# Performance work log

Measured on AMD Instinct MI355X. Metric: run time of the kernel, lower is better.

The kernel has to match this reference:

```python
import jax, jax.numpy as jnp
import numpy as np

B = 16          # graphs
NPG = 8192      # nodes per graph
N = B * NPG     # 131072 total nodes
E = 524288      # edges
F_NODE = 16
F_EDGE = 4
D = 128         # hidden_dim
OUT = 4
L = 3           # num_gnn_layers
K = 4096        # ceil(0.5 * NPG) nodes kept by SAGPooling
EPS = 1e-5


def setup_inputs() -> dict:
    key = jax.random.key(0)
    ks = jax.random.split(key, 24)
    # node / edge features
    x = jax.random.normal(ks[0], (N, F_NODE), jnp.float32)
    edge_attr = jax.random.normal(ks[1], (E, F_EDGE), jnp.float32)
    # edges constrained within each graph (nodes ordered by graph)
    gid = jax.random.randint(ks[2], (E,), 0, B)
    src = jax.random.randint(ks[3], (E,), 0, NPG) + gid * NPG
    dst = jax.random.randint(ks[4], (E,), 0, NPG) + gid * NPG
    edge_index = jnp.stack([src, dst]).astype(jnp.int32)

    def lin(k, fi, fo):
        kw, kb = jax.random.split(k)
        s = 1.0 / np.sqrt(fi)
        return (jax.random.uniform(kw, (fi, fo), jnp.float32, -s, s),
                jax.random.uniform(kb, (fo,), jnp.float32, -s, s))

    node_w, node_b = lin(ks[5], F_NODE, D)
    ew, eb = lin(ks[6], F_EDGE, D)
    conv_w = jax.random.normal(ks[7], (L, D, D), jnp.float32) / np.sqrt(D)
    conv_b = jnp.zeros((L, D), jnp.float32)
    bn_g = jnp.ones((L, D), jnp.float32)
    bn_b = jnp.zeros((L, D), jnp.float32)
    bn_m = jax.random.normal(ks[8], (L, D), jnp.float32) * 0.1
    bn_v = jax.random.uniform(ks[9], (L, D), jnp.float32, 0.5, 1.5)
    pool_wr, _ = lin(ks[10], D, 1)   # GraphConv lin_rel (neighbors)
    pool_ws, pool_b = lin(ks[11], D, 1)  # GraphConv lin_root (self) + bias
    r1_w, r1_b = lin(ks[12], D, D // 2)
    r2_w, r2_b = lin(ks[13], D // 2, OUT)
    return dict(x=x, edge_attr=edge_attr, edge_index=edge_index,
                node_w=node_w, node_b=node_b, ew=ew, eb=eb,
                conv_w=conv_w, conv_b=conv_b, bn_g=bn_g, bn_b=bn_b,
                bn_m=bn_m, bn_v=bn_v,
                pool_wr=pool_wr, pool_ws=pool_ws, pool_b=pool_b,
                r1_w=r1_w, r1_b=r1_b, r2_w=r2_w, r2_b=r2_b)


def reference(x, edge_attr, edge_index, node_w, node_b, ew, eb,
              conv_w, conv_b, bn_g, bn_b, bn_m, bn_v,
              pool_wr, pool_ws, pool_b, r1_w, r1_b, r2_w, r2_b):
    src, dst = edge_index[0], edge_index[1]
    # edge embedding (computed, but unused by GCNConv — faithful to source)
    _ea = jax.nn.leaky_relu(edge_attr @ ew + eb)
    h = x @ node_w + node_b                              # [N, D]
    # gcn_norm with self-loops: deg = 1 + in-degree
    deg = jax.ops.segment_sum(jnp.ones(E, h.dtype), dst, N) + 1.0
    dis = jax.lax.rsqrt(deg)                             # [N]
    coef = dis[src] * dis[dst]                           # [E]
    for i in range(L):
        hw = h @ conv_w[i]                               # [N, D]
        agg = jax.ops.segment_sum(hw[src] * coef[:, None], dst, N)
        h = agg + hw * (dis * dis)[:, None] + conv_b[i]  # GCNConv
        # BatchNorm (eval mode: running stats)
        h = (h - bn_m[i]) * jax.lax.rsqrt(bn_v[i] + EPS) * bn_g[i] + bn_b[i]
        h = jax.nn.leaky_relu(h)
        # dropout in eval mode = identity
    # SAGPooling: score via GraphConv(D, 1), aggr='add', nonlinearity=tanh
    nagg = jax.ops.segment_sum(h[src], dst, N)           # sum over neighbors
    score = (nagg @ pool_wr + h @ pool_ws + pool_b).reshape(N)
    top_vals, top_idx = jax.lax.top_k(score.reshape(B, NPG), K)  # per graph
    hb = h.reshape(B, NPG, D)
    hp = jnp.take_along_axis(hb, top_idx[..., None], axis=1)
    hp = hp * jnp.tanh(top_vals)[..., None]              # [B, K, D]
    xg = hp.sum(axis=1)                                  # global_add_pool [B, D]
    out = jax.nn.leaky_relu(xg @ r1_w + r1_b) @ r2_w + r2_b
    return out                                           # [B, OUT]
```

## Files before the change

### kernel.cpp

```cpp
#include <hip/hip_runtime.h>

#define N_NODES 131072
#define E_EDGES 524288
#define NGRAPH  16
#define NPG     8192
#define DIM     128
#define KSEL    4096
#define SCAN_BLOCKS 128

typedef float v2f __attribute__((ext_vector_type(2)));
typedef float v4f __attribute__((ext_vector_type(4)));

__global__ void count_deg_kernel(const int* __restrict__ ei, int* __restrict__ deg) {
    int e = blockIdx.x * 256 + threadIdx.x;
    atomicAdd(&deg[ei[E_EDGES + e]], 1);
}

__global__ __launch_bounds__(256) void scan_partial_kernel(const int* __restrict__ deg,
                                                           int* __restrict__ bsum) {
    __shared__ int wsh[4];
    int b = blockIdx.x, t = threadIdx.x;
    int4 v = ((const int4*)&deg[b * 1024])[t];
    int s = v.x + v.y + v.z + v.w;
#pragma unroll
    for (int off = 32; off; off >>= 1) s += __shfl_xor(s, off);
    if ((t & 63) == 0) wsh[t >> 6] = s;
    __syncthreads();
    if (t == 0) bsum[b] = wsh[0] + wsh[1] + wsh[2] + wsh[3];
}

__global__ __launch_bounds__(128) void scan_bsum_kernel(const int* __restrict__ bsum,
                                                        int* __restrict__ boff,
                                                        int* __restrict__ rowptr) {
    __shared__ int w0;
    int t = threadIdx.x;
    int lane = t & 63;
    int v = bsum[t];
    int x = v;
#pragma unroll
    for (int off = 1; off < 64; off <<= 1) {
        int y = __shfl_up(x, off);
        if (lane >= off) x += y;
    }
    if (t == 63) w0 = x;
    __syncthreads();
    int incl = x + ((t >= 64) ? w0 : 0);
    boff[t] = incl - v;
    if (t == 127) rowptr[N_NODES] = incl;
}

__global__ __launch_bounds__(256) void scan_final_kernel(const int* __restrict__ deg,
                                                         const int* __restrict__ boff,
                                                         int* __restrict__ rowptr,
                                                         int* __restrict__ cursor,
                                                         float* __restrict__ dis) {
    __shared__ int wsum[4];
    int b = blockIdx.x, t = threadIdx.x;
    int lane = t & 63, wv = t >> 6;
    int4 v = ((const int4*)&deg[b * 1024])[t];
    int s = v.x + v.y + v.z + v.w;
    int x = s;
#pragma unroll
    for (int off = 1; off < 64; off <<= 1) {
        int y = __shfl_up(x, off);
        if (lane >= off) x += y;
    }
    if (lane == 63) wsum[wv] = x;
    __syncthreads();
    int add = boff[b];
#pragma unroll
    for (int j = 0; j < 4; ++j)
        if (j < wv) add += wsum[j];
    int excl = add + (x - s);
    int base = b * 1024 + t * 4;
    int4 rp;
    rp.x = excl;
    rp.y = excl + v.x;
    rp.z = rp.y + v.y;
    rp.w = rp.z + v.z;
    *(int4*)&rowptr[base] = rp;
    *(int4*)&cursor[base] = rp;
    float4 dv;
    dv.x = rsqrtf((float)v.x + 1.0f);
    dv.y = rsqrtf((float)v.y + 1.0f);
    dv.z = rsqrtf((float)v.z + 1.0f);
    dv.w = rsqrtf((float)v.w + 1.0f);
    *(float4*)&dis[base] = dv;
}

__global__ void fill_csr_kernel(const int* __restrict__ ei, int* __restrict__ cursor,
                                const float* __restrict__ dis, int* __restrict__ csr_src,
                                float* __restrict__ csr_coef) {
    int e = blockIdx.x * 256 + threadIdx.x;
    int s = ei[e];
    int d = ei[E_EDGES + e];
    int p = atomicAdd(&cursor[d], 1);
    csr_src[p] = s;
    csr_coef[p] = dis[s] * dis[d];
}

__global__ __launch_bounds__(256) void embed_kernel(const float* __restrict__ x,
                                                    const float* __restrict__ nw,
                                                    const float* __restrict__ nb,
                                                    float* __restrict__ h) {
    __shared__ float Wl[16 * DIM];
    int t = threadIdx.x;
    for (int i = t * 4; i < 16 * DIM; i += 1024)
        *(float4*)&Wl[i] = *(const float4*)&nw[i];
    __syncthreads();
    int xslot = blockIdx.x & 7, q = blockIdx.x >> 3;
    int g = xslot + ((q >= 256) ? 8 : 0);
    int chunk = q & 255;
    int base = g * NPG + chunk * 32;
    int d = t & 127, sub = t >> 7;
    float bias = nb[d];
    for (int k = 0; k < 16; ++k) {
        int n = base + k * 2 + sub;
        const float* xr = &x[n * 16];
        float acc = bias;
#pragma unroll
        for (int f = 0; f < 16; ++f) acc += xr[f] * Wl[f * DIM + d];
        h[n * DIM + d] = acc;
    }
}

__global__ __launch_bounds__(256) void agg_kernel(const float* __restrict__ h,
                                                  const int* __restrict__ rowptr,
                                                  const int* __restrict__ csr_src,
                                                  const float* __restrict__ csr_coef,
                                                  const float* __restrict__ dis,
                                                  float* __restrict__ m) {
    int bb = blockIdx.x;
    int xslot = bb & 7;
    int c = bb >> 3;
    int g = xslot + ((c >= 512) ? 8 : 0);
    int chunk = c & 511;
    int t = threadIdx.x;
    int nl = t >> 6, l = t & 63;
    int nbase = g * NPG + chunk * 16;
#pragma unroll
    for (int it = 0; it < 4; ++it) {
        int n = nbase + it * 4 + nl;
        float dn = dis[n];
        float2 hv = *(const float2*)&h[(size_t)n * DIM + l * 2];
        float ax = dn * dn * hv.x;
        float ay = dn * dn * hv.y;
        int e0 = rowptr[n], e1 = rowptr[n + 1];
        int e = e0;
        for (; e + 4 <= e1; e += 4) {
            int s0 = csr_src[e],     s1 = csr_src[e + 1];
            int s2 = csr_src[e + 2], s3 = csr_src[e + 3];
            float c0 = csr_coef[e],     c1 = csr_coef[e + 1];
            float c2 = csr_coef[e + 2], c3 = csr_coef[e + 3];
            float2 v0 = *(const float2*)&h[(size_t)s0 * DIM + l * 2];
            float2 v1 = *(const float2*)&h[(size_t)s1 * DIM + l * 2];
            float2 v2 = *(const float2*)&h[(size_t)s2 * DIM + l * 2];
            float2 v3 = *(const float2*)&h[(size_t)s3 * DIM + l * 2];
            ax = fmaf(c0, v0.x, fmaf(c1, v1.x, fmaf(c2, v2.x, fmaf(c3, v3.x, ax))));
            ay = fmaf(c0, v0.y, fmaf(c1, v1.y, fmaf(c2, v2.y, fmaf(c3, v3.y, ay))));
        }
        for (; e < e1; ++e) {
            int s = csr_src[e];
            float cf = csr_coef[e];
            float2 v = *(const float2*)&h[(size_t)s * DIM + l * 2];
            ax = fmaf(cf, v.x, ax);
            ay = fmaf(cf, v.y, ay);
        }
        float2 o;
        o.x = ax; o.y = ay;
        *(float2*)&m[(size_t)n * DIM + l * 2] = o;
    }
}

__global__ __launch_bounds__(256, 2) void gemm_bn_kernel(const float* __restrict__ m,
                                                         const float* __restrict__ W,
                                                         const float* __restrict__ cb,
                                                         const float* __restrict__ bg,
                                                         const float* __restrict__ bb,
                                                         const float* __restrict__ bm,
                                                         const float* __restrict__ bv,
                                                         float* __restrict__ h,
                                                         const float* __restrict__ wr,
                                                         const float* __restrict__ ws,
                                                         const float* __restrict__ pb,
                                                         float* __restrict__ tb,
                                                         float* __restrict__ sb,
                                                         int fuse_dots) {
    __shared__ float Wl[DIM * DIM];
    v4f* Wl4 = (v4f*)Wl;
    const int t = threadIdx.x;
    const int i = t >> 4;
    const int j = t & 15;
    const int xslot = blockIdx.x & 7, q = blockIdx.x >> 3;
    const int graph = xslot + ((q >= 64) ? 8 : 0);
    const int chunk = q & 63;
    const int blockbase = graph * NPG + chunk * 128;

    {
        const v4f* W4 = (const v4f*)W;
#pragma unroll
        for (int p = 0; p < 16; ++p) {
            int idx = t + p * 256;
            int row = idx >> 5, c = idx & 31;
            Wl4[(row << 5) | ((c & 1) * 16 + (c >> 1))] = W4[idx];
        }
    }
    float A[8], C[8];
#pragma unroll
    for (int c = 0; c < 8; ++c) {
        int d = j * 8 + c;
        float inv = rsqrtf(bv[d] + 1e-5f);
        float a = bg[d] * inv;
        A[c] = a;
        C[c] = (cb[d] - bm[d]) * a + bb[d];
    }
    float wrf[8], wsf[8];
    float pb0 = 0.f;
    if (fuse_dots) {
        *(float4*)&wrf[0] = ((const float4*)wr)[j * 2];
        *(float4*)&wrf[4] = ((const float4*)wr)[j * 2 + 1];
        *(float4*)&wsf[0] = ((const float4*)ws)[j * 2];
        *(float4*)&wsf[4] = ((const float4*)ws)[j * 2 + 1];
        pb0 = pb[0];
    }
    __syncthreads();

    const float* mrow = &m[(size_t)(blockbase + i * 8) * DIM];

    float acc[8][8] = {{0.f}};
    v4f a0[8], a1[8];
#pragma unroll
    for (int r = 0; r < 8; ++r)
        a0[r] = *(const v4f*)&mrow[r * DIM];

    for (int k4 = 0; k4 < 32; k4 += 2) {
#pragma unroll
        for (int r = 0; r < 8; ++r)
            a1[r] = *(const v4f*)&mrow[r * DIM + (k4 + 1) * 4];
        {
            v4f bq[8];
#pragma unroll
            for (int u = 0; u < 4; ++u) {
                bq[u * 2]     = Wl4[(k4 * 4 + u) * 32 + j];
                bq[u * 2 + 1] = Wl4[(k4 * 4 + u) * 32 + 16 + j];
            }
#pragma unroll
            for (int u = 0; u < 4; ++u)
#pragma unroll
                for (int r = 0; r < 8; ++r) {
                    float av = a0[r][u];
#pragma unroll
                    for (int c = 0; c < 8; ++c)
                        acc[r][c] = fmaf(av, bq[u * 2 + (c >> 2)][c & 3], acc[r][c]);
                }
        }
        if (k4 < 30) {
#pragma unroll
            for (int r = 0; r < 8; ++r)
                a0[r] = *(const v4f*)&mrow[r * DIM + (k4 + 2) * 4];
        }
        {
            v4f bq[8];
#pragma unroll
            for (int u = 0; u < 4; ++u) {
                bq[u * 2]     = Wl4[((k4 + 1) * 4 + u) * 32 + j];
                bq[u * 2 + 1] = Wl4[((k4 + 1) * 4 + u) * 32 + 16 + j];
            }
#pragma unroll
            for (int u = 0; u < 4; ++u)
#pragma unroll
                for (int r = 0; r < 8; ++r) {
                    float av = a1[r][u];
#pragma unroll
                    for (int c = 0; c < 8; ++c)
                        acc[r][c] = fmaf(av, bq[u * 2 + (c >> 2)][c & 3], acc[r][c]);
                }
        }
    }

#pragma unroll
    for (int r = 0; r < 8; ++r) {
        int n = blockbase + i * 8 + r;
        float o[8];
#pragma unroll
        for (int c = 0; c < 8; ++c) {
            float y = acc[r][c] * A[c] + C[c];
            o[c] = y > 0.f ? y : 0.01f * y;
        }
        *(float4*)&h[(size_t)n * DIM + j * 8]     = *(float4*)&o[0];
        *(float4*)&h[(size_t)n * DIM + j * 8 + 4] = *(float4*)&o[4];
        if (fuse_dots) {
            float tr = 0.f, ts = 0.f;
#pragma unroll
            for (int c = 0; c < 8; ++c) {
                tr = fmaf(o[c], wrf[c], tr);
                ts = fmaf(o[c], wsf[c], ts);
            }
#pragma unroll
            for (int off = 1; off < 16; off <<= 1) {
                tr += __shfl_xor(tr, off);
                ts += __shfl_xor(ts, off);
            }
            if (j == 0) {
                tb[n] = tr;
                sb[n] = ts + pb0;
            }
        }
    }
}

__global__ void score_kernel(const int* __restrict__ rowptr, const int* __restrict__ csr_src,
                             const float* __restrict__ tb, float* __restrict__ sb) {
    int n = blockIdx.x * 256 + threadIdx.x;
    float s = sb[n];
    int e0 = rowptr[n], e1 = rowptr[n + 1];
    int e = e0;
    for (; e + 4 <= e1; e += 4) {
        float t0 = tb[csr_src[e]];
        float t1 = tb[csr_src[e + 1]];
        float t2 = tb[csr_src[e + 2]];
        float t3 = tb[csr_src[e + 3]];
        s += (t0 + t1) + (t2 + t3);
    }
    for (; e < e1; ++e) s += tb[csr_src[e]];
    sb[n] = s;
}

__global__ __launch_bounds__(256) void select_kernel(const float* __restrict__ sb,
                                                     float* __restrict__ wsel) {
    __shared__ unsigned su[NPG];
    __shared__ int hist[256];
    __shared__ int wsum[4];
    __shared__ unsigned pref_sh;
    __shared__ int kneed_sh;

    int b = blockIdx.x, t = threadIdx.x;
    int lane = t & 63, wv = t >> 6;
    const float* sc = &sb[b * NPG];
    for (int i = t; i < NPG; i += 256) {
        unsigned u = __float_as_uint(sc[i]);
        u = (u & 0x80000000u) ? ~u : (u | 0x80000000u);
        su[i] = u;
    }
    if (t == 0) { pref_sh = 0u; kneed_sh = KSEL; }
    __syncthreads();

    for (int p = 3; p >= 0; --p) {
        hist[t] = 0;
        __syncthreads();
        unsigned pref = pref_sh;
        int kneed = kneed_sh;
        int shift = p * 8;
        unsigned maskHi = (p == 3) ? 0u : (0xFFFFFFFFu << (shift + 8));
        for (int i = t; i < NPG; i += 256) {
            unsigned u = su[i];
            if ((u & maskHi) == (pref & maskHi))
                atomicAdd(&hist[(u >> shift) & 0xFFu], 1);
        }
        __syncthreads();
        int x = hist[t];
#pragma unroll
        for (int off = 1; off < 64; off <<= 1) {
            int y = __shfl_up(x, off);
            if (lane >= off) x += y;
        }
        if (lane == 63) wsum[wv] = x;
        __syncthreads();
        int add = 0, tot = 0;
#pragma unroll
        for (int jj = 0; jj < 4; ++jj) {
            int v = wsum[jj];
            tot += v;
            if (jj < wv) add += v;
        }
        int psum = x + add;
        int cnt_gt = tot - psum;
        int myh = hist[t];
        __syncthreads();
        if (cnt_gt < kneed && cnt_gt + myh >= kneed) {
            pref_sh = (pref & maskHi) | ((unsigned)t << shift);
            kneed_sh = kneed - cnt_gt;
        }
        __syncthreads();
    }
    unsigned T = pref_sh;
    int need_eq = kneed_sh;

    int base = t * 32;
    int local = 0;
#pragma unroll
    for (int k = 0; k < 32; ++k) local += (su[base + k] == T) ? 1 : 0;
    int x = local;
#pragma unroll
    for (int off = 1; off < 64; off <<= 1) {
        int y = __shfl_up(x, off);
        if (lane >= off) x += y;
    }
    if (lane == 63) wsum[wv] = x;
    __syncthreads();
    int add = 0;
#pragma unroll
    for (int jj = 0; jj < 4; ++jj)
        if (jj < wv) add += wsum[jj];
    int rank = (x - local) + add;
#pragma unroll
    for (int k = 0; k < 32; ++k) {
        unsigned u = su[base + k];
        bool take = (u > T);
        if (u == T) { take = (rank < need_eq); ++rank; }
        float w = 0.f;
        if (take) {
            float f = (u & 0x80000000u) ? __uint_as_float(u & 0x7FFFFFFFu)
                                        : __uint_as_float(~u);
            w = tanhf(f);
        }
        wsel[b * NPG + base + k] = w;
    }
}

__global__ __launch_bounds__(256) void pool_kernel(const float* __restrict__ wsel,
                                                   const float* __restrict__ h,
                                                   float* __restrict__ part) {
    int xslot = blockIdx.x & 7, q = blockIdx.x >> 3;
    int b = xslot + ((q >= 32) ? 8 : 0);
    int ch = q & 31;
    int t = threadIdx.x;
    int nl = t >> 6;
    int l = t & 63;
    int n0 = b * NPG + ch * 256;
    float ax = 0.f, ay = 0.f;
    for (int i = nl; i < 256; i += 4) {
        int n = n0 + i;
        float w = wsel[n];
        if (w != 0.f) {
            float2 v = *(const float2*)&h[(size_t)n * DIM + l * 2];
            ax += w * v.x;
            ay += w * v.y;
        }
    }
    __shared__ float pp[4][DIM];
    pp[nl][l * 2] = ax;
    pp[nl][l * 2 + 1] = ay;
    __syncthreads();
    if (t < DIM) {
        float s = pp[0][t] + pp[1][t] + pp[2][t] + pp[3][t];
        part[((size_t)b * 32 + ch) * DIM + t] = s;
    }
}

__global__ void pool_reduce_kernel(const float* __restrict__ part,
                                   float* __restrict__ xg) {
    int b = blockIdx.x, d = threadIdx.x;
    float s = 0.f;
    for (int c = 0; c < 32; ++c) s += part[((size_t)b * 32 + c) * DIM + d];
    xg[b * DIM + d] = s;
}

__global__ __launch_bounds__(1024) void mlp_kernel(const float* __restrict__ xg,
                                                   const float* __restrict__ r1w,
                                                   const float* __restrict__ r1b,
                                                   const float* __restrict__ r2w,
                                                   const float* __restrict__ r2b,
                                                   float* __restrict__ out) {
    __shared__ float h1[16 * 64];
    int t = threadIdx.x;
    {
        int b = t >> 6, j = t & 63;
        float acc = r1b[j];
        for (int k = 0; k < DIM; ++k) acc += xg[b * DIM + k] * r1w[k * 64 + j];
        h1[b * 64 + j] = acc > 0.f ? acc : 0.01f * acc;
    }
    __syncthreads();
    if (t < 64) {
        int b = t >> 2, o = t & 3;
        float acc = r2b[o];
        for (int k = 0; k < 64; ++k) acc += h1[b * 64 + k] * r2w[k * 4 + o];
        out[b * 4 + o] = acc;
    }
}

extern "C" void kernel_launch(void* const* d_in, const int* in_sizes, int n_in,
                              void* d_out, int out_size, void* d_ws, size_t ws_size,
                              hipStream_t stream) {
    const float* x       = (const float*)d_in[0];
    const int*   ei      = (const int*)d_in[2];
    const float* node_w  = (const float*)d_in[3];
    const float* node_b  = (const float*)d_in[4];
    const float* conv_w  = (const float*)d_in[7];
    const float* conv_b  = (const float*)d_in[8];
    const float* bn_g    = (const float*)d_in[9];
    const float* bn_b    = (const float*)d_in[10];
    const float* bn_m    = (const float*)d_in[11];
    const float* bn_v    = (const float*)d_in[12];
    const float* pool_wr = (const float*)d_in[13];
    const float* pool_ws = (const float*)d_in[14];
    const float* pool_b  = (const float*)d_in[15];
    const float* r1_w    = (const float*)d_in[16];
    const float* r1_b    = (const float*)d_in[17];
    const float* r2_w    = (const float*)d_in[18];
    const float* r2_b    = (const float*)d_in[19];
    float* out = (float*)d_out;

    char* ws = (char*)d_ws;
    size_t off = 0;
    auto alloc = [&](size_t bytes) {
        void* p = ws + off;
        off = (off + bytes + 255) & ~(size_t)255;
        return p;
    };
    float* h       = (float*)alloc((size_t)N_NODES * DIM * 4);
    float* mbuf    = (float*)alloc((size_t)N_NODES * DIM * 4);
    int*   deg     = (int*)alloc((size_t)N_NODES * 4);
    int*   rowptr  = (int*)alloc((size_t)(N_NODES + 1) * 4);
    int*   cursor  = (int*)alloc((size_t)N_NODES * 4);
    float* dis     = (float*)alloc((size_t)N_NODES * 4);
    int*   csr_src = (int*)alloc((size_t)E_EDGES * 4);
    float* csr_cf  = (float*)alloc((size_t)E_EDGES * 4);
    float* tb      = (float*)alloc((size_t)N_NODES * 4);
    float* sb      = (float*)alloc((size_t)N_NODES * 4);
    float* wsel    = (float*)alloc((size_t)N_NODES * 4);
    float* part    = (float*)alloc((size_t)NGRAPH * 32 * DIM * 4);
    float* xg      = (float*)alloc((size_t)NGRAPH * DIM * 4);
    int*   bsum    = (int*)alloc((size_t)SCAN_BLOCKS * 4);
    int*   boff    = (int*)alloc((size_t)SCAN_BLOCKS * 4);

    hipMemsetAsync(deg, 0, (size_t)N_NODES * 4, stream);
    count_deg_kernel<<<E_EDGES / 256, 256, 0, stream>>>(ei, deg);
    scan_partial_kernel<<<SCAN_BLOCKS, 256, 0, stream>>>(deg, bsum);
    scan_bsum_kernel<<<1, 128, 0, stream>>>(bsum, boff, rowptr);
    scan_final_kernel<<<SCAN_BLOCKS, 256, 0, stream>>>(deg, boff, rowptr, cursor, dis);
    fill_csr_kernel<<<E_EDGES / 256, 256, 0, stream>>>(ei, cursor, dis, csr_src, csr_cf);
    embed_kernel<<<N_NODES / 32, 256, 0, stream>>>(x, node_w, node_b, h);

    for (int layer = 0; layer < 3; ++layer) {
        agg_kernel<<<8192, 256, 0, stream>>>(h, rowptr, csr_src, csr_cf, dis, mbuf);
        gemm_bn_kernel<<<N_NODES / 128, 256, 0, stream>>>(
            mbuf, conv_w + (size_t)layer * DIM * DIM, conv_b + layer * DIM,
            bn_g + layer * DIM, bn_b + layer * DIM, bn_m + layer * DIM,
            bn_v + layer * DIM, h,
            pool_wr, pool_ws, pool_b, tb, sb, (layer == 2) ? 1 : 0);
    }

    score_kernel<<<N_NODES / 256, 256, 0, stream>>>(rowptr, csr_src, tb, sb);
    select_kernel<<<NGRAPH, 256, 0, stream>>>(sb, wsel);
    pool_kernel<<<NGRAPH * 32, 256, 0, stream>>>(wsel, h, part);
    pool_reduce_kernel<<<NGRAPH, DIM, 0, stream>>>(part, xg);
    mlp_kernel<<<1, 1024, 0, stream>>>(xg, r1_w, r1_b, r2_w, r2_b, out);
}
```

Before: 489.9 us.

## Fuse neighbor aggregation and GEMM+BN into one per-layer kernel

Merges the CSR aggregation kernel and the dense GEMM/BatchNorm/LeakyReLU kernel into one kernel per layer. Each block aggregates 32 nodes into a swizzled LDS tile, then multiplies that tile by W held in LDS. This removes the write and re-read of the full intermediate message buffer in global memory, and h now ping-pongs between two buffers. In exchange, the 64KB weight matrix is reloaded for every 32-node block instead of every 128 nodes. The larger LDS footprint also limits occupancy during the latency-bound gather phase.

```diff
diff --git a/kernel.cpp b/kernel.cpp
--- a/kernel.cpp
+++ b/kernel.cpp
@@ -124,95 +124,93 @@
     }
 }
 
-__global__ __launch_bounds__(256) void agg_kernel(const float* __restrict__ h,
-                                                  const int* __restrict__ rowptr,
-                                                  const int* __restrict__ csr_src,
-                                                  const float* __restrict__ csr_coef,
-                                                  const float* __restrict__ dis,
-                                                  float* __restrict__ m) {
-    int bb = blockIdx.x;
-    int xslot = bb & 7;
-    int c = bb >> 3;
-    int g = xslot + ((c >= 512) ? 8 : 0);
-    int chunk = c & 511;
-    int t = threadIdx.x;
-    int nl = t >> 6, l = t & 63;
-    int nbase = g * NPG + chunk * 16;
-#pragma unroll
-    for (int it = 0; it < 4; ++it) {
-        int n = nbase + it * 4 + nl;
-        float dn = dis[n];
-        float2 hv = *(const float2*)&h[(size_t)n * DIM + l * 2];
-        float ax = dn * dn * hv.x;
-        float ay = dn * dn * hv.y;
-        int e0 = rowptr[n], e1 = rowptr[n + 1];
-        int e = e0;
-        for (; e + 4 <= e1; e += 4) {
-            int s0 = csr_src[e],     s1 = csr_src[e + 1];
-            int s2 = csr_src[e + 2], s3 = csr_src[e + 3];
-            float c0 = csr_coef[e],     c1 = csr_coef[e + 1];
-            float c2 = csr_coef[e + 2], c3 = csr_coef[e + 3];
-            float2 v0 = *(const float2*)&h[(size_t)s0 * DIM + l * 2];
-            float2 v1 = *(const float2*)&h[(size_t)s1 * DIM + l * 2];
-            float2 v2 = *(const float2*)&h[(size_t)s2 * DIM + l * 2];
-            float2 v3 = *(const float2*)&h[(size_t)s3 * DIM + l * 2];
-            ax = fmaf(c0, v0.x, fmaf(c1, v1.x, fmaf(c2, v2.x, fmaf(c3, v3.x, ax))));
-            ay = fmaf(c0, v0.y, fmaf(c1, v1.y, fmaf(c2, v2.y, fmaf(c3, v3.y, ay))));
-        }
-        for (; e < e1; ++e) {
-            int s = csr_src[e];
-            float cf = csr_coef[e];
-            float2 v = *(const float2*)&h[(size_t)s * DIM + l * 2];
-            ax = fmaf(cf, v.x, ax);
-            ay = fmaf(cf, v.y, ay);
-        }
-        float2 o;
-        o.x = ax; o.y = ay;
-        *(float2*)&m[(size_t)n * DIM + l * 2] = o;
-    }
-}
-
-__global__ __launch_bounds__(256, 2) void gemm_bn_kernel(const float* __restrict__ m,
-                                                         const float* __restrict__ W,
-                                                         const float* __restrict__ cb,
-                                                         const float* __restrict__ bg,
-                                                         const float* __restrict__ bb,
-                                                         const float* __restrict__ bm,
-                                                         const float* __restrict__ bv,
-                                                         float* __restrict__ h,
-                                                         const float* __restrict__ wr,
-                                                         const float* __restrict__ ws,
-                                                         const float* __restrict__ pb,
-                                                         float* __restrict__ tb,
-                                                         float* __restrict__ sb,
-                                                         int fuse_dots) {
+__global__ __launch_bounds__(256, 2) void fused_layer_kernel(
+        const float* __restrict__ hin,
+        const int* __restrict__ rowptr,
+        const int* __restrict__ csr_src,
+        const float* __restrict__ csr_coef,
+        const float* __restrict__ dis,
+        const float* __restrict__ W,
+        const float* __restrict__ cb,
+        const float* __restrict__ bg,
+        const float* __restrict__ bb,
+        const float* __restrict__ bm,
+        const float* __restrict__ bv,
+        float* __restrict__ hout,
+        const float* __restrict__ wr,
+        const float* __restrict__ ws,
+        const float* __restrict__ pb,
+        float* __restrict__ tb,
+        float* __restrict__ sb,
+        int fuse_dots) {
     __shared__ float Wl[DIM * DIM];
+    __shared__ float Ml[32 * DIM];
     v4f* Wl4 = (v4f*)Wl;
+    v4f* Ml4 = (v4f*)Ml;
     const int t = threadIdx.x;
+    const int xslot = blockIdx.x & 7, c = blockIdx.x >> 3;
+    const int g = xslot + ((c >= 256) ? 8 : 0);
+    const int chunk = c & 255;
+    const int nbase = g * NPG + chunk * 32;
+
+    {
+        const v4f* W4 = (const v4f*)W;
+#pragma unroll
+        for (int p = 0; p < 16; ++p) {
+            int idx = t + p * 256;
+            int row = idx >> 5, cc = idx & 31;
+            Wl4[(row << 5) | ((cc & 1) * 16 + (cc >> 1))] = W4[idx];
+        }
+    }
+
+    {
+        int wv = t >> 6, l = t & 63;
+        for (int k = 0; k < 8; ++k) {
+            int nodeLocal = wv * 8 + k;
+            int n = nbase + nodeLocal;
+            float dn = dis[n];
+            float2 hv = *(const float2*)&hin[(size_t)n * DIM + l * 2];
+            float ax = dn * dn * hv.x;
+            float ay = dn * dn * hv.y;
+            int e0 = rowptr[n], e1 = rowptr[n + 1];
+            int e = e0;
+            for (; e + 4 <= e1; e += 4) {
+                int s0 = csr_src[e],     s1 = csr_src[e + 1];
+                int s2 = csr_src[e + 2], s3 = csr_src[e + 3];
+                float c0 = csr_coef[e],     c1 = csr_coef[e + 1];
+                float c2 = csr_coef[e + 2], c3 = csr_coef[e + 3];
+                float2 v0 = *(const float2*)&hin[(size_t)s0 * DIM + l * 2];
+                float2 v1 = *(const float2*)&hin[(size_t)s1 * DIM + l * 2];
+                float2 v2 = *(const float2*)&hin[(size_t)s2 * DIM + l * 2];
+                float2 v3 = *(const float2*)&hin[(size_t)s3 * DIM + l * 2];
+                ax = fmaf(c0, v0.x, fmaf(c1, v1.x, fmaf(c2, v2.x, fmaf(c3, v3.x, ax))));
+                ay = fmaf(c0, v0.y, fmaf(c1, v1.y, fmaf(c2, v2.y, fmaf(c3, v3.y, ay))));
+            }
+            for (; e < e1; ++e) {
+                int s = csr_src[e];
+                float cf = csr_coef[e];
+                float2 v = *(const float2*)&hin[(size_t)s * DIM + l * 2];
+                ax = fmaf(cf, v.x, ax);
+                ay = fmaf(cf, v.y, ay);
+            }
+            int slot = (l >> 1) ^ nodeLocal;
+            float2 o; o.x = ax; o.y = ay;
+            *(float2*)&Ml[nodeLocal * DIM + slot * 4 + (l & 1) * 2] = o;
+        }
+    }
+    __syncthreads();
+
     const int i = t >> 4;
     const int j = t & 15;
-    const int xslot = blockIdx.x & 7, q = blockIdx.x >> 3;
-    const int graph = xslot + ((q >= 64) ? 8 : 0);
-    const int chunk = q & 63;
-    const int blockbase = graph * NPG + chunk * 128;
-
-    {
-        const v4f* W4 = (const v4f*)W;
-#pragma unroll
-        for (int p = 0; p < 16; ++p) {
-            int idx = t + p * 256;
-            int row = idx >> 5, c = idx & 31;
-            Wl4[(row << 5) | ((c & 1) * 16 + (c >> 1))] = W4[idx];
-        }
-    }
+    const int r0 = i * 2, r1 = i * 2 + 1;
     float A[8], C[8];
 #pragma unroll
-    for (int c = 0; c < 8; ++c) {
-        int d = j * 8 + c;
+    for (int cc = 0; cc < 8; ++cc) {
+        int d = j * 8 + cc;
         float inv = rsqrtf(bv[d] + 1e-5f);
         float a = bg[d] * inv;
-        A[c] = a;
-        C[c] = (cb[d] - bm[d]) * a + bb[d];
+        A[cc] = a;
+        C[cc] = (cb[d] - bm[d]) * a + bb[d];
     }
     float wrf[8], wsf[8];
     float pb0 = 0.f;
@@ -223,78 +221,47 @@
         *(float4*)&wsf[4] = ((const float4*)ws)[j * 2 + 1];
         pb0 = pb[0];
     }
-    __syncthreads();
-
-    const float* mrow = &m[(size_t)(blockbase + i * 8) * DIM];
-
-    float acc[8][8] = {{0.f}};
-    v4f a0[8], a1[8];
-#pragma unroll
-    for (int r = 0; r < 8; ++r)
-        a0[r] = *(const v4f*)&mrow[r * DIM];
-
-    for (int k4 = 0; k4 < 32; k4 += 2) {
-#pragma unroll
-        for (int r = 0; r < 8; ++r)
-            a1[r] = *(const v4f*)&mrow[r * DIM + (k4 + 1) * 4];
-        {
-            v4f bq[8];
-#pragma unroll
-            for (int u = 0; u < 4; ++u) {
-                bq[u * 2]     = Wl4[(k4 * 4 + u) * 32 + j];
-                bq[u * 2 + 1] = Wl4[(k4 * 4 + u) * 32 + 16 + j];
+
+    float acc0[8] = {0.f, 0.f, 0.f, 0.f, 0.f, 0.f, 0.f, 0.f};
+    float acc1[8] = {0.f, 0.f, 0.f, 0.f, 0.f, 0.f, 0.f, 0.f};
+    for (int k4 = 0; k4 < 32; ++k4) {
+        v4f a0 = Ml4[r0 * 32 + (k4 ^ r0)];
+        v4f a1 = Ml4[r1 * 32 + (k4 ^ r1)];
+        v4f bq[8];
+#pragma unroll
+        for (int u = 0; u < 4; ++u) {
+            bq[u * 2]     = Wl4[(k4 * 4 + u) * 32 + j];
+            bq[u * 2 + 1] = Wl4[(k4 * 4 + u) * 32 + 16 + j];
+        }
+#pragma unroll
+        for (int u = 0; u < 4; ++u) {
+            float av0 = a0[u], av1 = a1[u];
+#pragma unroll
+            for (int cc = 0; cc < 8; ++cc) {
+                float w = bq[u * 2 + (cc >> 2)][cc & 3];
+                acc0[cc] = fmaf(av0, w, acc0[cc]);
+                acc1[cc] = fmaf(av1, w, acc1[cc]);
             }
-#pragma unroll
-            for (int u = 0; u < 4; ++u)
-#pragma unroll
-                for (int r = 0; r < 8; ++r) {
-                    float av = a0[r][u];
-#pragma unroll
-                    for (int c = 0; c < 8; ++c)
-                        acc[r][c] = fmaf(av, bq[u * 2 + (c >> 2)][c & 3], acc[r][c]);
-                }
-        }
-        if (k4 < 30) {
-#pragma unroll
-            for (int r = 0; r < 8; ++r)
-                a0[r] = *(const v4f*)&mrow[r * DIM + (k4 + 2) * 4];
-        }
-        {
-            v4f bq[8];
-#pragma unroll
-            for (int u = 0; u < 4; ++u) {
-                bq[u * 2]     = Wl4[((k4 + 1) * 4 + u) * 32 + j];
-                bq[u * 2 + 1] = Wl4[((k4 + 1) * 4 + u) * 32 + 16 + j];
-            }
-#pragma unroll
-            for (int u = 0; u < 4; ++u)
-#pragma unroll
-                for (int r = 0; r < 8; ++r) {
-                    float av = a1[r][u];
-#pragma unroll
-                    for (int c = 0; c < 8; ++c)
-                        acc[r][c] = fmaf(av, bq[u * 2 + (c >> 2)][c & 3], acc[r][c]);
-                }
-        }
-    }
-
-#pragma unroll
-    for (int r = 0; r < 8; ++r) {
-        int n = blockbase + i * 8 + r;
+        }
+    }
+
+#pragma unroll
+    for (int r = 0; r < 2; ++r) {
+        int n = nbase + i * 2 + r;
         float o[8];
 #pragma unroll
-        for (int c = 0; c < 8; ++c) {
-            float y = acc[r][c] * A[c] + C[c];
-            o[c] = y > 0.f ? y : 0.01f * y;
-        }
-        *(float4*)&h[(size_t)n * DIM + j * 8]     = *(float4*)&o[0];
-        *(float4*)&h[(size_t)n * DIM + j * 8 + 4] = *(float4*)&o[4];
+        for (int cc = 0; cc < 8; ++cc) {
+            float y = (r == 0 ? acc0[cc] : acc1[cc]) * A[cc] + C[cc];
+            o[cc] = y > 0.f ? y : 0.01f * y;
+        }
+        *(float4*)&hout[(size_t)n * DIM + j * 8]     = *(float4*)&o[0];
+        *(float4*)&hout[(size_t)n * DIM + j * 8 + 4] = *(float4*)&o[4];
         if (fuse_dots) {
             float tr = 0.f, ts = 0.f;
 #pragma unroll
-            for (int c = 0; c < 8; ++c) {
-                tr = fmaf(o[c], wrf[c], tr);
-                ts = fmaf(o[c], wsf[c], ts);
+            for (int cc = 0; cc < 8; ++cc) {
+                tr = fmaf(o[cc], wrf[cc], tr);
+                ts = fmaf(o[cc], wsf[cc], ts);
             }
 #pragma unroll
             for (int off = 1; off < 16; off <<= 1) {
@@ -508,8 +475,8 @@
         off = (off + bytes + 255) & ~(size_t)255;
         return p;
     };
-    float* h       = (float*)alloc((size_t)N_NODES * DIM * 4);
-    float* mbuf    = (float*)alloc((size_t)N_NODES * DIM * 4);
+    float* hA      = (float*)alloc((size_t)N_NODES * DIM * 4);
+    float* hB      = (float*)alloc((size_t)N_NODES * DIM * 4);
     int*   deg     = (int*)alloc((size_t)N_NODES * 4);
     int*   rowptr  = (int*)alloc((size_t)(N_NODES + 1) * 4);
     int*   cursor  = (int*)alloc((size_t)N_NODES * 4);
@@ -530,20 +497,26 @@
     scan_bsum_kernel<<<1, 128, 0, stream>>>(bsum, boff, rowptr);
     scan_final_kernel<<<SCAN_BLOCKS, 256, 0, stream>>>(deg, boff, rowptr, cursor, dis);
     fill_csr_kernel<<<E_EDGES / 256, 256, 0, stream>>>(ei, cursor, dis, csr_src, csr_cf);
-    embed_kernel<<<N_NODES / 32, 256, 0, stream>>>(x, node_w, node_b, h);
-
+    embed_kernel<<<N_NODES / 32, 256, 0, stream>>>(x, node_w, node_b, hA);
+
+    const float* hin = hA;
+    float* hout = hB;
     for (int layer = 0; layer < 3; ++layer) {
-        agg_kernel<<<8192, 256, 0, stream>>>(h, rowptr, csr_src, csr_cf, dis, mbuf);
-        gemm_bn_kernel<<<N_NODES / 128, 256, 0, stream>>>(
-            mbuf, conv_w + (size_t)layer * DIM * DIM, conv_b + layer * DIM,
+        fused_layer_kernel<<<N_NODES / 32, 256, 0, stream>>>(
+            hin, rowptr, csr_src, csr_cf, dis,
+            conv_w + (size_t)layer * DIM * DIM, conv_b + layer * DIM,
             bn_g + layer * DIM, bn_b + layer * DIM, bn_m + layer * DIM,
-            bn_v + layer * DIM, h,
+            bn_v + layer * DIM, hout,
             pool_wr, pool_ws, pool_b, tb, sb, (layer == 2) ? 1 : 0);
-    }
+        const float* tmp = hin;
+        hin = hout;
+        hout = (float*)tmp;
+    }
+    const float* hfinal = hB;
 
     score_kernel<<<N_NODES / 256, 256, 0, stream>>>(rowptr, csr_src, tb, sb);
     select_kernel<<<NGRAPH, 256, 0, stream>>>(sb, wsel);
-    pool_kernel<<<NGRAPH * 32, 256, 0, stream>>>(wsel, h, part);
+    pool_kernel<<<NGRAPH * 32, 256, 0, stream>>>(wsel, hfinal, part);
     pool_reduce_kernel<<<NGRAPH, DIM, 0, stream>>>(part, xg);
     mlp_kernel<<<1, 1024, 0, stream>>>(xg, r1_w, r1_b, r2_w, r2_b, out);
 }
```

Result: slower. 632.8 us (+29.1%).
